# Kernel tuning notes

Hardware: AMD Instinct MI355X
Metric: run time of the kernel (lower is better)

Reference implementation:

```python
import jax, jax.numpy as jnp
import numpy as np

B, T, DIM, H = 2, 2048, 1024, 16
DH = DIM // H  # head dim = 64, rope half = 32


def _apply_rope(q, k):
    # q,k: [b,h,t,d]
    b, h, t, d = q.shape
    half = d // 2
    idx = jnp.arange(half, dtype=jnp.float32)
    pos = jnp.arange(t, dtype=jnp.float32)[:, None]
    inv = 10000.0 ** (-2.0 * idx / (2.0 * half))
    ang = pos * inv  # [t, half]
    cos = jnp.cos(ang).astype(q.dtype)[None, None]  # [1,1,t,half]
    sin = jnp.sin(ang).astype(q.dtype)[None, None]

    def rot(x):
        a = x[..., :half]
        b2 = x[..., half:2 * half]
        return jnp.concatenate([a * cos - b2 * sin, a * sin + b2 * cos], axis=-1)

    return rot(q), rot(k)


def setup_inputs() -> dict:
    key = jax.random.key(0)
    k0, k1, k2 = jax.random.split(key, 3)
    x = jax.random.normal(k0, (B, T, DIM), dtype=jnp.float32)
    mask = jnp.tril(jnp.ones((T, T), dtype=jnp.int32))[None, None]  # causal [1,1,T,T]
    scale = DIM ** -0.5
    W_qkv = jax.random.normal(k1, (DIM, 3 * DIM), dtype=jnp.float32) * scale
    b_qkv = jnp.zeros((3 * DIM,), dtype=jnp.float32)
    W_out = jax.random.normal(k2, (DIM, DIM), dtype=jnp.float32) * scale
    b_out = jnp.zeros((DIM,), dtype=jnp.float32)
    return {"x": x, "mask": mask, "W_qkv": W_qkv, "b_qkv": b_qkv,
            "W_out": W_out, "b_out": b_out}


def reference(x, mask, W_qkv, b_qkv, W_out, b_out):
    b, t, c = x.shape
    qkv = x @ W_qkv + b_qkv  # [b,t,3c]
    q, k, v = jnp.split(qkv, 3, axis=-1)
    q = q.reshape(b, t, H, DH).transpose(0, 2, 1, 3)  # [b,h,t,dh]
    k = k.reshape(b, t, H, DH).transpose(0, 2, 1, 3)
    v = v.reshape(b, t, H, DH).transpose(0, 2, 1, 3)
    q, k = _apply_rope(q, k)
    s = jnp.einsum('bhqd,bhkd->bhqk', q, k) * (DH ** -0.5)
    s = jnp.where(mask == 0, -jnp.inf, s)
    p = jax.nn.softmax(s, axis=-1)  # dropout is identity (drop=0.0)
    y = jnp.einsum('bhqk,bhkd->bhqd', p, v)
    y = y.transpose(0, 2, 1, 3).reshape(b, t, c)
    return y @ W_out + b_out
```

## Files before the change

### kernel.cpp

```cpp
#include <hip/hip_runtime.h>
#include <hip/hip_bf16.h>
#include <math.h>

#define BB 2
#define TT 2048
#define DIMM 1024
#define HH 16
#define DHH 64

typedef _Float16 half8_t __attribute__((ext_vector_type(8)));
typedef _Float16 half4_t __attribute__((ext_vector_type(4)));
typedef float floatx4 __attribute__((ext_vector_type(4)));

typedef const unsigned int __attribute__((address_space(1)))* gp_t;
typedef unsigned int __attribute__((address_space(3)))* lp_t;

__device__ __forceinline__ void async16(const void* g, void* l) {
    __builtin_amdgcn_global_load_lds((gp_t)g, (lp_t)l, 16, 0, 0);
}

template <int CTRL>
__device__ __forceinline__ float dppmov(float x) {
    return __builtin_bit_cast(float, __builtin_amdgcn_update_dpp(
        0, __builtin_bit_cast(int, x), CTRL, 0xf, 0xf, false));
}
__device__ __forceinline__ float rowred_sum(float v) {
    v += dppmov<0x128>(v);
    v += dppmov<0x124>(v);
    v += dppmov<0x122>(v);
    v += dppmov<0x121>(v);
    return v;
}

__global__ __launch_bounds__(256) void prep_kernel(
    const float* __restrict__ x, _Float16* __restrict__ xb,
    const float* __restrict__ W_qkv, _Float16* __restrict__ Wqt,
    const float* __restrict__ W_out, _Float16* __restrict__ Wot,
    float2* __restrict__ tab) {
    __shared__ float tile[32][33];
    int bid = blockIdx.x, tid = threadIdx.x;
    if (bid < 4096) {
        int i = (bid * 256 + tid) * 4;
        floatx4 v = *(const floatx4*)(x + i);
        half4_t h;
        h[0] = (_Float16)v[0]; h[1] = (_Float16)v[1];
        h[2] = (_Float16)v[2]; h[3] = (_Float16)v[3];
        *(half4_t*)(xb + i) = h;
    } else if (bid < 8192) {
        const float* W; _Float16* Wt; int K, N, bx, by;
        if (bid < 7168) {
            W = W_qkv; Wt = Wqt; K = 1024; N = 3072;
            int b2 = bid - 4096; bx = b2 % 96; by = b2 / 96;
        } else {
            W = W_out; Wt = Wot; K = 1024; N = 1024;
            int b2 = bid - 7168; bx = b2 & 31; by = b2 >> 5;
        }
        int n0 = bx * 32, k0 = by * 32;
        int tx = tid & 31, ty = tid >> 5;
        for (int i = 0; i < 32; i += 8)
            tile[ty + i][tx] = W[(size_t)(k0 + ty + i) * N + n0 + tx];
        __syncthreads();
        for (int i = 0; i < 32; i += 8)
            Wt[(size_t)(n0 + ty + i) * K + k0 + tx] = (_Float16)tile[tx][ty + i];
    } else {
        int idx = (bid - 8192) * 256 + tid;
        int t = idx >> 5, d = idx & 31;
        float inv = __expf(-(float)d * 0.28782313662425572f);
        float ang = (float)t * inv;
        float s, c;
        __sincosf(ang, &s, &c);
        tab[idx] = make_float2(c, s);
    }
}

template <int BN, int MODE>
__global__ __launch_bounds__(256) void gemm_ld_kernel(
    const _Float16* __restrict__ A, const _Float16* __restrict__ Bt,
    const float* __restrict__ bias, float* __restrict__ C,
    _Float16* __restrict__ Qr, _Float16* __restrict__ Kr, _Float16* __restrict__ Vt,
    const float2* __restrict__ tab,
    int M, int N, int K) {
    constexpr int NB = (BN == 128) ? 4 : 2;
    __shared__ __align__(16) _Float16 As[2][128 * 32];
    __shared__ __align__(16) _Float16 Bs[2][BN * 32];
    int tid = threadIdx.x;
    int m0 = blockIdx.y * 128, n0 = blockIdx.x * BN;
    int wave = tid >> 6, lane = tid & 63;
    int wm = (wave & 1) * 64;
    int wn = (wave >> 1) * (BN / 2);
    int lm = lane & 15, quad = lane >> 4;

    floatx4 acc[4][NB] = {};

    int srow = tid >> 2;
    int scol = (tid & 3) * 8;

    auto stage = [&](int k0, int buf) {
        const _Float16* g0 = A + (size_t)(m0 + srow) * K + k0 + scol;
        async16(g0, (char*)&As[buf][0] + (wave * 64) * 16);
        const _Float16* g1 = A + (size_t)(m0 + 64 + srow) * K + k0 + scol;
        async16(g1, (char*)&As[buf][0] + (256 + wave * 64) * 16);
        const _Float16* gb0 = Bt + (size_t)(n0 + srow) * K + k0 + scol;
        async16(gb0, (char*)&Bs[buf][0] + (wave * 64) * 16);
        if (BN == 128) {
            const _Float16* gb1 = Bt + (size_t)(n0 + 64 + srow) * K + k0 + scol;
            async16(gb1, (char*)&Bs[buf][0] + (256 + wave * 64) * 16);
        }
    };

    int nIt = K >> 5;
    stage(0, 0);
    for (int it = 0; it < nIt; ++it) {
        int buf = it & 1;
        __syncthreads();
        if (it + 1 < nIt) stage((it + 1) << 5, buf ^ 1);

        half8_t af[4], bf[NB];
        for (int mb = 0; mb < 4; mb++)
            af[mb] = *(const half8_t*)&As[buf][(wm + mb * 16 + lm) * 32 + quad * 8];
        for (int nb = 0; nb < NB; nb++)
            bf[nb] = *(const half8_t*)&Bs[buf][(wn + nb * 16 + lm) * 32 + quad * 8];
        for (int mb = 0; mb < 4; mb++)
            for (int nb = 0; nb < NB; nb++)
                acc[mb][nb] = __builtin_amdgcn_mfma_f32_16x16x32_f16(af[mb], bf[nb], acc[mb][nb], 0, 0, 0);
    }

    if (MODE == 0) {
        for (int mb = 0; mb < 4; mb++) {
            int row = m0 + wm + mb * 16 + quad * 4;
            for (int nb = 0; nb < NB; nb++) {
                int col = n0 + wn + nb * 16 + lm;
                float bv = bias[col];
                for (int r = 0; r < 4; r++)
                    C[(size_t)(row + r) * N + col] = acc[mb][nb][r] + bv;
            }
        }
    } else {
        int col0 = n0 + wn;
        int sect = col0 >> 10;
        int h = (col0 & 1023) >> 6;
        if (sect < 2) {
            _Float16* dst = (sect == 0) ? Qr : Kr;
            float fscale = (sect == 0) ? 0.18033688011112042f : 1.0f;
            for (int nb = 0; nb < 2; nb++) {
                int d = nb * 16 + lm;
                float bva = bias[col0 + d];
                float bvb = bias[col0 + d + 32];
                for (int mb = 0; mb < 4; mb++) {
                    int row = m0 + wm + mb * 16 + quad * 4;
                    int b = row >> 11;
                    size_t ob0 = ((size_t)(b * HH + h) * TT) * 64;
                    for (int r = 0; r < 4; r++) {
                        int t = (row + r) & 2047;
                        float2 cs = tab[t * 32 + d];
                        float va = acc[mb][nb][r] + bva;
                        float vb = acc[mb][nb + 2][r] + bvb;
                        size_t ob = ob0 + (size_t)t * 64;
                        dst[ob + d] = (_Float16)((va * cs.x - vb * cs.y) * fscale);
                        dst[ob + d + 32] = (_Float16)((va * cs.y + vb * cs.x) * fscale);
                    }
                }
            }
        } else {
            for (int nb = 0; nb < 4; nb++) {
                int d = nb * 16 + lm;
                float bv = bias[col0 + d];
                for (int mb = 0; mb < 4; mb++) {
                    int row = m0 + wm + mb * 16 + quad * 4;
                    int b = row >> 11;
                    int t = row & 2047;
                    half4_t pv;
                    for (int r = 0; r < 4; r++) pv[r] = (_Float16)(acc[mb][nb][r] + bv);
                    *(half4_t*)&Vt[((size_t)(b * HH + h) * 64 + d) * TT + t] = pv;
                }
            }
        }
    }
}

__device__ const unsigned char kBlkMap[24] = {
    30, 28, 26, 24, 22, 20, 18, 16, 14, 31,
    12, 29, 10, 27, 8, 25, 6, 23, 4, 21, 2, 19, 0, 17};

__global__ __launch_bounds__(256, 3) void flash_attn(
    const _Float16* __restrict__ Qr, const _Float16* __restrict__ Kr,
    const _Float16* __restrict__ Vt,
    _Float16* __restrict__ Po, float* __restrict__ Pls) {
    int bh = blockIdx.y;
    int code = kBlkMap[blockIdx.x];
    int iq = code >> 1, ic = code & 1;
    int kstart = ic * 16;
    int kend = min(kstart + 16, 2 * iq + 2);

    int tid = threadIdx.x, wave = tid >> 6, lane = tid & 63;
    int lm = lane & 15, quad = lane >> 4;
    int q0w = iq * 128 + wave * 32;

    __shared__ __align__(16) _Float16 Ks[2][64 * 64];
    __shared__ __align__(16) _Float16 Vs[2][64 * 64];
    __shared__ __align__(16) _Float16 Pbuf[4][32 * 64];
    _Float16* plds = Pbuf[wave];

    const _Float16* Qbase = Qr + ((size_t)bh * TT + q0w) * 64;
    half8_t aq[2][2];
    for (int mb = 0; mb < 2; mb++) {
        aq[mb][0] = *(const half8_t*)(Qbase + (size_t)(mb * 16 + lm) * 64 + quad * 8);
        aq[mb][1] = *(const half8_t*)(Qbase + (size_t)(mb * 16 + lm) * 64 + 32 + quad * 8);
    }

    const _Float16* Kb = Kr + (size_t)bh * TT * 64;
    const _Float16* Vb = Vt + (size_t)bh * 64 * TT;

    floatx4 o[2][4] = {};
    float lsum[2][4] = {};

    auto stage = [&](int kt, int buf) {
        int k0 = kt * 64;
        for (int i = 0; i < 2; i++) {
            int sl = i * 256 + tid;
            int row = sl >> 3;
            int c = (sl & 7) ^ (row & 7);
            async16(Kb + (size_t)(k0 + row) * 64 + c * 8, (char*)&Ks[buf][0] + sl * 16);
            async16(Vb + (size_t)row * TT + k0 + c * 8, (char*)&Vs[buf][0] + sl * 16);
        }
    };

    stage(kstart, 0);

    for (int kt = kstart; kt < kend; ++kt) {
        int buf = (kt - kstart) & 1;
        __syncthreads();
        if (kt + 1 < kend) stage(kt + 1, buf ^ 1);
        int k0 = kt * 64;
        if (k0 > q0w + 31) continue;

        floatx4 s4[2][4] = {};
        for (int nb = 0; nb < 4; nb++) {
            int row = nb * 16 + lm, sw = row & 7;
            half8_t kb0 = *(const half8_t*)&Ks[buf][row * 64 + ((quad ^ sw) << 3)];
            half8_t kb1 = *(const half8_t*)&Ks[buf][row * 64 + (((4 + quad) ^ sw) << 3)];
            for (int mb = 0; mb < 2; mb++) {
                s4[mb][nb] = __builtin_amdgcn_mfma_f32_16x16x32_f16(aq[mb][0], kb0, s4[mb][nb], 0, 0, 0);
                s4[mb][nb] = __builtin_amdgcn_mfma_f32_16x16x32_f16(aq[mb][1], kb1, s4[mb][nb], 0, 0, 0);
            }
        }

        if (k0 + 63 > q0w) {
            for (int mb = 0; mb < 2; mb++)
                for (int nb = 0; nb < 4; nb++) {
                    int col = k0 + nb * 16 + lm;
                    int rowq = q0w + mb * 16 + quad * 4;
                    for (int r = 0; r < 4; r++)
                        if (col > rowq + r) s4[mb][nb][r] = -1e30f;
                }
        }

        for (int mb = 0; mb < 2; mb++)
            for (int nb = 0; nb < 4; nb++) {
                int cbase = nb * 2 + (lm >> 3);
                for (int r = 0; r < 4; r++) {
                    float p = __builtin_amdgcn_exp2f(s4[mb][nb][r]);
                    lsum[mb][r] += p;
                    int prow = mb * 16 + quad * 4 + r;
                    plds[prow * 64 + ((cbase ^ (prow & 7)) << 3) + (lm & 7)] = (_Float16)p;
                }
            }
        asm volatile("s_waitcnt lgkmcnt(0)" ::: "memory");
        int psw = lm & 7;
        half8_t pa[2][2];
        for (int mp = 0; mp < 2; mp++) {
            pa[mp][0] = *(const half8_t*)&plds[(mp * 16 + lm) * 64 + ((quad ^ psw) << 3)];
            pa[mp][1] = *(const half8_t*)&plds[(mp * 16 + lm) * 64 + (((4 + quad) ^ psw) << 3)];
        }
        asm volatile("" ::: "memory");

        for (int db = 0; db < 4; db++) {
            int row = db * 16 + lm, sw = row & 7;
            half8_t vb0 = *(const half8_t*)&Vs[buf][row * 64 + ((quad ^ sw) << 3)];
            half8_t vb1 = *(const half8_t*)&Vs[buf][row * 64 + (((4 + quad) ^ sw) << 3)];
            for (int mb = 0; mb < 2; mb++) {
                o[mb][db] = __builtin_amdgcn_mfma_f32_16x16x32_f16(pa[mb][0], vb0, o[mb][db], 0, 0, 0);
                o[mb][db] = __builtin_amdgcn_mfma_f32_16x16x32_f16(pa[mb][1], vb1, o[mb][db], 0, 0, 0);
            }
        }
    }

    float lred[2][4];
    for (int mb = 0; mb < 2; mb++)
        for (int r = 0; r < 4; r++)
            lred[mb][r] = rowred_sum(lsum[mb][r]);

    size_t pbase = ((size_t)(bh * 16 + iq) * 2 + ic) * 8192;
    for (int mb = 0; mb < 2; mb++)
        for (int db = 0; db < 4; db++)
            for (int r = 0; r < 4; r++) {
                int row = wave * 32 + mb * 16 + quad * 4 + r;
                Po[pbase + row * 64 + db * 16 + lm] = (_Float16)o[mb][db][r];
            }
    if (lm == 0) {
        size_t lb = ((size_t)(bh * 16 + iq) * 2 + ic) * 128;
        for (int mb = 0; mb < 2; mb++)
            for (int r = 0; r < 4; r++)
                Pls[lb + wave * 32 + mb * 16 + quad * 4 + r] = lred[mb][r];
    }
}

__global__ __launch_bounds__(256) void attn_combine(
    const _Float16* __restrict__ Po, const float* __restrict__ Pls,
    _Float16* __restrict__ Yb) {
    int iq = blockIdx.x, bh = blockIdx.y;
    int b = bh >> 4, h = bh & 15;
    int tid = threadIdx.x;
    int row = tid >> 1, cg = (tid & 1) * 32;

    size_t base = ((size_t)(bh * 16 + iq) * 2) * 8192 + row * 64 + cg;
    size_t lb = ((size_t)(bh * 16 + iq) * 2) * 128 + row;
    float l = Pls[lb];
    float acc[32];
    {
        const half8_t* p = (const half8_t*)&Po[base];
        for (int j = 0; j < 4; j++) {
            half8_t v = p[j];
            for (int i = 0; i < 8; i++) acc[j * 8 + i] = (float)v[i];
        }
    }
    if (iq >= 8) {
        l += Pls[lb + 128];
        const half8_t* p = (const half8_t*)&Po[base + 8192];
        for (int j = 0; j < 4; j++) {
            half8_t v = p[j];
            for (int i = 0; i < 8; i++) acc[j * 8 + i] += (float)v[i];
        }
    }
    float inv = 1.0f / l;
    size_t yb = ((size_t)(b * TT) + iq * 128 + row) * DIMM + h * 64 + cg;
    for (int j = 0; j < 4; j++) {
        half8_t v;
        for (int i = 0; i < 8; i++) v[i] = (_Float16)(acc[j * 8 + i] * inv);
        *(half8_t*)&Yb[yb + j * 8] = v;
    }
}

extern "C" void kernel_launch(void* const* d_in, const int* in_sizes, int n_in,
                              void* d_out, int out_size, void* d_ws, size_t ws_size,
                              hipStream_t stream) {
    const float* x = (const float*)d_in[0];
    const float* W_qkv = (const float*)d_in[2];
    const float* b_qkv = (const float*)d_in[3];
    const float* W_out = (const float*)d_in[4];
    const float* b_out = (const float*)d_in[5];
    float* out = (float*)d_out;

    char* ws = (char*)d_ws;
    _Float16* xb = (_Float16*)ws;   ws += (size_t)4096 * 1024 * 2;
    _Float16* Wqt = (_Float16*)ws;  ws += (size_t)3072 * 1024 * 2;
    _Float16* Wot = (_Float16*)ws;  ws += (size_t)1024 * 1024 * 2;
    _Float16* Qr = (_Float16*)ws;   ws += (size_t)32 * 2048 * 64 * 2;
    _Float16* Kr = (_Float16*)ws;   ws += (size_t)32 * 2048 * 64 * 2;
    _Float16* Vt = (_Float16*)ws;   ws += (size_t)32 * 2048 * 64 * 2;
    _Float16* Yb = (_Float16*)ws;   ws += (size_t)4096 * 1024 * 2;
    float2* tab = (float2*)ws;      ws += (size_t)2048 * 32 * 8;
    _Float16* Po = (_Float16*)ws;   ws += (size_t)32 * 16 * 2 * 8192 * 2;
    float* Pls = (float*)ws;        ws += (size_t)32 * 16 * 2 * 128 * 4;

    prep_kernel<<<8448, 256, 0, stream>>>(x, xb, W_qkv, Wqt, W_out, Wot, tab);

    gemm_ld_kernel<128, 1><<<dim3(24, 32), 256, 0, stream>>>(
        xb, Wqt, b_qkv, nullptr, Qr, Kr, Vt, tab, 4096, 3072, 1024);

    flash_attn<<<dim3(24, 32), 256, 0, stream>>>(Qr, Kr, Vt, Po, Pls);
    attn_combine<<<dim3(16, 32), 256, 0, stream>>>(Po, Pls, Yb);

    gemm_ld_kernel<64, 0><<<dim3(16, 32), 256, 0, stream>>>(
        Yb, Wot, b_out, out, nullptr, nullptr, nullptr, nullptr, 4096, 1024, 1024);
}
```

Before: 205.9 us.

## Triple-buffer GEMM with swizzled LDS, stage epilogues via LDS, fuse unsplit attention normalize

```diff
diff --git a/kernel.cpp b/kernel.cpp
--- a/kernel.cpp
+++ b/kernel.cpp
@@ -81,8 +81,9 @@
     const float2* __restrict__ tab,
     int M, int N, int K) {
     constexpr int NB = (BN == 128) ? 4 : 2;
-    __shared__ __align__(16) _Float16 As[2][128 * 32];
-    __shared__ __align__(16) _Float16 Bs[2][BN * 32];
+    constexpr int BCH = BN * 32;
+    constexpr int BOFF = 3 * 4096;
+    __shared__ __align__(16) _Float16 smem[3 * 4096 + 3 * BCH];
     int tid = threadIdx.x;
     int m0 = blockIdx.y * 128, n0 = blockIdx.x * BN;
     int wave = tid >> 6, lane = tid & 63;
@@ -92,34 +93,41 @@
 
     floatx4 acc[4][NB] = {};
 
-    int srow = tid >> 2;
-    int scol = (tid & 3) * 8;
+    int arow = tid >> 2, ach = tid & 3;
+    int acol = ((ach ^ (arow & 3)) << 3);
 
     auto stage = [&](int k0, int buf) {
-        const _Float16* g0 = A + (size_t)(m0 + srow) * K + k0 + scol;
-        async16(g0, (char*)&As[buf][0] + (wave * 64) * 16);
-        const _Float16* g1 = A + (size_t)(m0 + 64 + srow) * K + k0 + scol;
-        async16(g1, (char*)&As[buf][0] + (256 + wave * 64) * 16);
-        const _Float16* gb0 = Bt + (size_t)(n0 + srow) * K + k0 + scol;
-        async16(gb0, (char*)&Bs[buf][0] + (wave * 64) * 16);
-        if (BN == 128) {
-            const _Float16* gb1 = Bt + (size_t)(n0 + 64 + srow) * K + k0 + scol;
-            async16(gb1, (char*)&Bs[buf][0] + (256 + wave * 64) * 16);
-        }
+        _Float16* Ab = smem + buf * 4096;
+        _Float16* Bb = smem + BOFF + buf * BCH;
+        async16(A + (size_t)(m0 + arow) * K + k0 + acol, (char*)Ab + tid * 16);
+        async16(A + (size_t)(m0 + 64 + arow) * K + k0 + acol, (char*)Ab + (256 + tid) * 16);
+        async16(Bt + (size_t)(n0 + arow) * K + k0 + acol, (char*)Bb + tid * 16);
+        if (BN == 128)
+            async16(Bt + (size_t)(n0 + 64 + arow) * K + k0 + acol, (char*)Bb + (256 + tid) * 16);
     };
 
     int nIt = K >> 5;
     stage(0, 0);
+    stage(32, 1);
+    int fsw = (quad ^ (lm & 3)) << 3;
     for (int it = 0; it < nIt; ++it) {
-        int buf = it & 1;
-        __syncthreads();
-        if (it + 1 < nIt) stage((it + 1) << 5, buf ^ 1);
-
+        int buf = it % 3;
+        if (it < nIt - 1) {
+            if (BN == 128) asm volatile("s_waitcnt vmcnt(4)" ::: "memory");
+            else           asm volatile("s_waitcnt vmcnt(3)" ::: "memory");
+        } else {
+            asm volatile("s_waitcnt vmcnt(0)" ::: "memory");
+        }
+        asm volatile("s_barrier" ::: "memory");
+        if (it + 2 < nIt) stage((it + 2) << 5, (it + 2) % 3);
+
+        const _Float16* Ab = smem + buf * 4096;
+        const _Float16* Bb = smem + BOFF + buf * BCH;
         half8_t af[4], bf[NB];
         for (int mb = 0; mb < 4; mb++)
-            af[mb] = *(const half8_t*)&As[buf][(wm + mb * 16 + lm) * 32 + quad * 8];
+            af[mb] = *(const half8_t*)&Ab[(wm + mb * 16 + lm) * 32 + fsw];
         for (int nb = 0; nb < NB; nb++)
-            bf[nb] = *(const half8_t*)&Bs[buf][(wn + nb * 16 + lm) * 32 + quad * 8];
+            bf[nb] = *(const half8_t*)&Bb[(wn + nb * 16 + lm) * 32 + fsw];
         for (int mb = 0; mb < 4; mb++)
             for (int nb = 0; nb < NB; nb++)
                 acc[mb][nb] = __builtin_amdgcn_mfma_f32_16x16x32_f16(af[mb], bf[nb], acc[mb][nb], 0, 0, 0);
@@ -136,9 +144,13 @@
             }
         }
     } else {
+        __syncthreads();
+        _Float16* scratch = smem + wave * 4096;
         int col0 = n0 + wn;
         int sect = col0 >> 10;
         int h = (col0 & 1023) >> 6;
+        int b = (m0 + wm) >> 11;
+        int tbase = (m0 + wm) & 2047;
         if (sect < 2) {
             _Float16* dst = (sect == 0) ? Qr : Kr;
             float fscale = (sect == 0) ? 0.18033688011112042f : 1.0f;
@@ -146,33 +158,48 @@
                 int d = nb * 16 + lm;
                 float bva = bias[col0 + d];
                 float bvb = bias[col0 + d + 32];
+                int d2 = d + 32;
                 for (int mb = 0; mb < 4; mb++) {
-                    int row = m0 + wm + mb * 16 + quad * 4;
-                    int b = row >> 11;
-                    size_t ob0 = ((size_t)(b * HH + h) * TT) * 64;
                     for (int r = 0; r < 4; r++) {
-                        int t = (row + r) & 2047;
-                        float2 cs = tab[t * 32 + d];
+                        int tl = mb * 16 + quad * 4 + r;
+                        float2 cs = tab[(tbase + tl) * 32 + d];
                         float va = acc[mb][nb][r] + bva;
                         float vb = acc[mb][nb + 2][r] + bvb;
-                        size_t ob = ob0 + (size_t)t * 64;
-                        dst[ob + d] = (_Float16)((va * cs.x - vb * cs.y) * fscale);
-                        dst[ob + d + 32] = (_Float16)((va * cs.y + vb * cs.x) * fscale);
+                        int sw = tl & 7;
+                        scratch[tl * 64 + (((d >> 3) ^ sw) << 3) + (d & 7)] =
+                            (_Float16)((va * cs.x - vb * cs.y) * fscale);
+                        scratch[tl * 64 + (((d2 >> 3) ^ sw) << 3) + (d2 & 7)] =
+                            (_Float16)((va * cs.y + vb * cs.x) * fscale);
                     }
                 }
+            }
+            asm volatile("s_waitcnt lgkmcnt(0)" ::: "memory");
+            size_t ob = (size_t)(b * HH + h) * TT + tbase;
+            for (int j = 0; j < 8; j++) {
+                int row = j * 8 + (lane >> 3);
+                int c = lane & 7;
+                half8_t v = *(const half8_t*)&scratch[row * 64 + ((c ^ (row & 7)) << 3)];
+                *(half8_t*)&dst[(ob + row) * 64 + c * 8] = v;
             }
         } else {
             for (int nb = 0; nb < 4; nb++) {
                 int d = nb * 16 + lm;
                 float bv = bias[col0 + d];
+                int sw = d & 7;
                 for (int mb = 0; mb < 4; mb++) {
-                    int row = m0 + wm + mb * 16 + quad * 4;
-                    int b = row >> 11;
-                    int t = row & 2047;
+                    int t0 = mb * 16 + quad * 4;
                     half4_t pv;
                     for (int r = 0; r < 4; r++) pv[r] = (_Float16)(acc[mb][nb][r] + bv);
-                    *(half4_t*)&Vt[((size_t)(b * HH + h) * 64 + d) * TT + t] = pv;
+                    *(half4_t*)&scratch[d * 64 + (((t0 >> 3) ^ sw) << 3) + (t0 & 7)] = pv;
                 }
+            }
+            asm volatile("s_waitcnt lgkmcnt(0)" ::: "memory");
+            size_t vb0 = (size_t)(b * HH + h) * 64;
+            for (int j = 0; j < 8; j++) {
+                int drow = j * 8 + (lane >> 3);
+                int c = lane & 7;
+                half8_t v = *(const half8_t*)&scratch[drow * 64 + ((c ^ (drow & 7)) << 3)];
+                *(half8_t*)&Vt[(vb0 + drow) * TT + tbase + c * 8] = v;
             }
         }
     }
@@ -185,12 +212,13 @@
 __global__ __launch_bounds__(256, 3) void flash_attn(
     const _Float16* __restrict__ Qr, const _Float16* __restrict__ Kr,
     const _Float16* __restrict__ Vt,
-    _Float16* __restrict__ Po, float* __restrict__ Pls) {
+    _Float16* __restrict__ Po, float* __restrict__ Pls, _Float16* __restrict__ Yb) {
     int bh = blockIdx.y;
     int code = kBlkMap[blockIdx.x];
     int iq = code >> 1, ic = code & 1;
     int kstart = ic * 16;
     int kend = min(kstart + 16, 2 * iq + 2);
+    bool full = (ic == 0) && (kend == 2 * iq + 2);
 
     int tid = threadIdx.x, wave = tid >> 6, lane = tid & 63;
     int lm = lane & 15, quad = lane >> 4;
@@ -290,14 +318,31 @@
         for (int r = 0; r < 4; r++)
             lred[mb][r] = rowred_sum(lsum[mb][r]);
 
+    for (int mb = 0; mb < 2; mb++)
+        for (int db = 0; db < 4; db++) {
+            int cbase = db * 2 + (lm >> 3);
+            for (int r = 0; r < 4; r++) {
+                int prow = mb * 16 + quad * 4 + r;
+                float v = o[mb][db][r];
+                if (full) v /= lred[mb][r];
+                plds[prow * 64 + ((cbase ^ (prow & 7)) << 3) + (lm & 7)] = (_Float16)v;
+            }
+        }
+    asm volatile("s_waitcnt lgkmcnt(0)" ::: "memory");
+    int b = bh >> 4, h = bh & 15;
     size_t pbase = ((size_t)(bh * 16 + iq) * 2 + ic) * 8192;
-    for (int mb = 0; mb < 2; mb++)
-        for (int db = 0; db < 4; db++)
-            for (int r = 0; r < 4; r++) {
-                int row = wave * 32 + mb * 16 + quad * 4 + r;
-                Po[pbase + row * 64 + db * 16 + lm] = (_Float16)o[mb][db][r];
-            }
-    if (lm == 0) {
+    for (int j = 0; j < 4; j++) {
+        int row = j * 8 + (lane >> 3);
+        int c = lane & 7;
+        half8_t v = *(const half8_t*)&plds[row * 64 + ((c ^ (row & 7)) << 3)];
+        if (full) {
+            size_t yb = ((size_t)(b * TT) + iq * 128 + wave * 32 + row) * DIMM + h * 64 + c * 8;
+            *(half8_t*)&Yb[yb] = v;
+        } else {
+            *(half8_t*)&Po[pbase + (wave * 32 + row) * 64 + c * 8] = v;
+        }
+    }
+    if (!full && lm == 0) {
         size_t lb = ((size_t)(bh * 16 + iq) * 2 + ic) * 128;
         for (int mb = 0; mb < 2; mb++)
             for (int r = 0; r < 4; r++)
@@ -308,35 +353,22 @@
 __global__ __launch_bounds__(256) void attn_combine(
     const _Float16* __restrict__ Po, const float* __restrict__ Pls,
     _Float16* __restrict__ Yb) {
-    int iq = blockIdx.x, bh = blockIdx.y;
+    int iq = blockIdx.x + 8, bh = blockIdx.y;
     int b = bh >> 4, h = bh & 15;
     int tid = threadIdx.x;
     int row = tid >> 1, cg = (tid & 1) * 32;
 
     size_t base = ((size_t)(bh * 16 + iq) * 2) * 8192 + row * 64 + cg;
     size_t lb = ((size_t)(bh * 16 + iq) * 2) * 128 + row;
-    float l = Pls[lb];
-    float acc[32];
-    {
-        const half8_t* p = (const half8_t*)&Po[base];
-        for (int j = 0; j < 4; j++) {
-            half8_t v = p[j];
-            for (int i = 0; i < 8; i++) acc[j * 8 + i] = (float)v[i];
-        }
-    }
-    if (iq >= 8) {
-        l += Pls[lb + 128];
-        const half8_t* p = (const half8_t*)&Po[base + 8192];
-        for (int j = 0; j < 4; j++) {
-            half8_t v = p[j];
-            for (int i = 0; i < 8; i++) acc[j * 8 + i] += (float)v[i];
-        }
-    }
+    float l = Pls[lb] + Pls[lb + 128];
     float inv = 1.0f / l;
+    const half8_t* p0 = (const half8_t*)&Po[base];
+    const half8_t* p1 = (const half8_t*)&Po[base + 8192];
     size_t yb = ((size_t)(b * TT) + iq * 128 + row) * DIMM + h * 64 + cg;
     for (int j = 0; j < 4; j++) {
-        half8_t v;
-        for (int i = 0; i < 8; i++) v[i] = (_Float16)(acc[j * 8 + i] * inv);
+        half8_t a = p0[j], c = p1[j], v;
+        for (int i = 0; i < 8; i++)
+            v[i] = (_Float16)(((float)a[i] + (float)c[i]) * inv);
         *(half8_t*)&Yb[yb + j * 8] = v;
     }
 }
@@ -368,8 +400,8 @@
     gemm_ld_kernel<128, 1><<<dim3(24, 32), 256, 0, stream>>>(
         xb, Wqt, b_qkv, nullptr, Qr, Kr, Vt, tab, 4096, 3072, 1024);
 
-    flash_attn<<<dim3(24, 32), 256, 0, stream>>>(Qr, Kr, Vt, Po, Pls);
-    attn_combine<<<dim3(16, 32), 256, 0, stream>>>(Po, Pls, Yb);
+    flash_attn<<<dim3(24, 32), 256, 0, stream>>>(Qr, Kr, Vt, Po, Pls, Yb);
+    attn_combine<<<dim3(8, 32), 256, 0, stream>>>(Po, Pls, Yb);
 
     gemm_ld_kernel<64, 0><<<dim3(16, 32), 256, 0, stream>>>(
         Yb, Wot, b_out, out, nullptr, nullptr, nullptr, nullptr, 4096, 1024, 1024);
```

Measured after the change: 194.4 us. 5.6% less time.
